# Optimization experiments

Measured on AMD Instinct MI355X. Metric: run time of the kernel, lower is better.

## Reference

```python
import jax, jax.numpy as jnp
import numpy as np

DIM, NH, HD = 1536, 12, 128
F, H, W = 1, 30, 52
SEQ = F * H * W          # 1560 tokens per AR group
NG, GI = 6, 5            # num_groups, group_idx (attend over full prefix)
POS, EPS = 1024, 1e-6


def _rope_table():
    # cos/sin table matching Wan rope_params: bands [c-2(c//3), c//3, c//3] of head_dim//2
    c = HD // 2
    parts = [c - 2 * (c // 3), c // 3, c // 3]
    pos = np.arange(POS, dtype=np.float64)
    angs = []
    for cp in parts:
        inv = 1.0 / (10000.0 ** (np.arange(cp, dtype=np.float64) / cp))
        angs.append(pos[:, None] * inv[None, :])
    ang = np.concatenate(angs, axis=1)  # [POS, c]
    return jnp.asarray(np.stack([np.cos(ang), np.sin(ang)], axis=-1), dtype=jnp.float32)


def setup_inputs() -> dict:
    key = jax.random.key(0)
    ks = jax.random.split(key, 8)
    lin = lambda k: jax.random.normal(k, (DIM, DIM), jnp.float32) * 0.02
    total = NG * SEQ
    return {
        'x': jax.random.normal(ks[0], (1, SEQ, DIM), jnp.float32),
        'wq': lin(ks[1]), 'bq': jnp.zeros((DIM,), jnp.float32),
        'wk': lin(ks[2]), 'bk': jnp.zeros((DIM,), jnp.float32),
        'wv': lin(ks[3]), 'bv': jnp.zeros((DIM,), jnp.float32),
        'wo': lin(ks[4]), 'bo': jnp.zeros((DIM,), jnp.float32),
        'nq_w': jnp.ones((DIM,), jnp.float32),
        'nk_w': jnp.ones((DIM,), jnp.float32),
        'freqs': _rope_table(),
        'k_cache': jax.random.normal(ks[5], (1, total, NH, HD), jnp.float32) * 0.5,
        'v_cache': jax.random.normal(ks[6], (1, total, NH, HD), jnp.float32) * 0.5,
        'f': F, 'h': H, 'w': W, 'group_idx': GI, 'num_groups': NG,
    }


def _rms_norm(x, weight, eps=EPS):
    # fast_rms_norm: normalize over the full channel dim, then scale
    x = x.astype(jnp.float32)
    return x * jax.lax.rsqrt(jnp.mean(x * x, axis=-1, keepdims=True) + eps) * weight


def _rope_apply(x, freqs, f, h, w, group_idx):
    # x: [B, S, N, D] with S = f*h*w; freqs: [POS, D//2, 2] (cos, sin)
    B, S, N, D = x.shape
    c = D // 2
    cf = c - 2 * (c // 3)
    ch = cw = c // 3
    sf = group_idx * f
    fp = jnp.broadcast_to(freqs[sf:sf + f, :cf][:, None, None], (f, h, w, cf, 2))
    hp = jnp.broadcast_to(freqs[:h, cf:cf + ch][None, :, None], (f, h, w, ch, 2))
    wp = jnp.broadcast_to(freqs[:w, cf + ch:][None, None, :], (f, h, w, cw, 2))
    rot = jnp.concatenate([fp, hp, wp], axis=3).reshape(S, c, 2)  # [S, c, 2]
    cos = rot[..., 0][None, :, None]  # [1, S, 1, c]
    sin = rot[..., 1][None, :, None]
    xr = x.astype(jnp.float32).reshape(B, S, N, c, 2)
    out_r = xr[..., 0] * cos - xr[..., 1] * sin  # complex multiply x * e^{i theta}
    out_i = xr[..., 0] * sin + xr[..., 1] * cos
    return jnp.stack([out_r, out_i], axis=-1).reshape(B, S, N, D)


def reference(x, wq, bq, wk, bk, wv, bv, wo, bo, nq_w, nk_w, freqs,
              k_cache, v_cache, f, h, w, group_idx, num_groups):
    B, S, C = x.shape
    n, d = NH, C // NH
    q = _rms_norm(x @ wq.T + bq, nq_w).reshape(B, S, n, d)
    k = _rms_norm(x @ wk.T + bk, nk_w).reshape(B, S, n, d)
    v = (x @ wv.T + bv).reshape(B, S, n, d)
    q = _rope_apply(q, freqs, f, h, w, group_idx)
    k = _rope_apply(k, freqs, f, h, w, group_idx)
    # KV-cache scatter (detached in the original) then prefix gather
    start = group_idx * S
    kc = jax.lax.dynamic_update_slice(k_cache, jax.lax.stop_gradient(k), (0, start, 0, 0))
    vc = jax.lax.dynamic_update_slice(v_cache, jax.lax.stop_gradient(v), (0, start, 0, 0))
    k_full = kc[:, :start + S]  # [B, Lkv, n, d]
    v_full = vc[:, :start + S]
    att = jnp.einsum('bqnd,bknd->bnqk', q, k_full) / jnp.sqrt(jnp.float32(d))
    p = jax.nn.softmax(att, axis=-1)
    o = jnp.einsum('bnqk,bknd->bqnd', p, v_full).reshape(B, S, C)
    return o @ wo.T + bo
```

## Files before the change

kernel.cpp:

```cpp
#include <hip/hip_runtime.h>

#define DIM 1536
#define NH 12
#define HD 128
#define KSPLIT 8
#define KT 32
#define MFIX 3.0f
#define KK48 48

typedef _Float16 half2_t __attribute__((ext_vector_type(2)));
typedef _Float16 half8_t __attribute__((ext_vector_type(8)));
typedef float f32x4 __attribute__((ext_vector_type(4)));

__device__ __forceinline__ half2_t pkrtz(float a, float b) {
    return __builtin_bit_cast(half2_t, __builtin_amdgcn_cvt_pkrtz(a, b));
}

__device__ __forceinline__ void split8(float4 a, float4 b, half8_t& h, half8_t& l) {
    half2_t h0 = pkrtz(a.x, a.y), h1 = pkrtz(a.z, a.w);
    half2_t h2 = pkrtz(b.x, b.y), h3 = pkrtz(b.z, b.w);
    half2_t g0 = pkrtz(a.x - (float)h0.x, a.y - (float)h0.y);
    half2_t g1 = pkrtz(a.z - (float)h1.x, a.w - (float)h1.y);
    half2_t g2 = pkrtz(b.x - (float)h2.x, b.y - (float)h2.y);
    half2_t g3 = pkrtz(b.z - (float)h3.x, b.w - (float)h3.y);
    h[0]=h0.x; h[1]=h0.y; h[2]=h1.x; h[3]=h1.y; h[4]=h2.x; h[5]=h2.y; h[6]=h3.x; h[7]=h3.y;
    l[0]=g0.x; l[1]=g0.y; l[2]=g1.x; l[3]=g1.y; l[4]=g2.x; l[5]=g2.y; l[6]=g3.x; l[7]=g3.y;
}

__device__ __forceinline__ half8_t cvt8rn(float4 a, float4 b) {
    half8_t h;
    h[0]=(_Float16)a.x; h[1]=(_Float16)a.y; h[2]=(_Float16)a.z; h[3]=(_Float16)a.w;
    h[4]=(_Float16)b.x; h[5]=(_Float16)b.y; h[6]=(_Float16)b.z; h[7]=(_Float16)b.w;
    return h;
}

__device__ __forceinline__ void gl2lds16(const void* g, void* l) {
    __builtin_amdgcn_global_load_lds(
        (const __attribute__((address_space(1))) unsigned int*)g,
        (__attribute__((address_space(3))) unsigned int*)(unsigned int)(uintptr_t)l,
        16, 0, 0);
}


__global__ __launch_bounds__(256) void cvt_a_fl(
    const float* __restrict__ src, _Float16* __restrict__ h, _Float16* __restrict__ l,
    int M, int nrec8)
{
    const int i = blockIdx.x * 256 + threadIdx.x;
    if (i >= nrec8) return;
    const int lane = i & 63;
    const int grp  = (i >> 6) & 7;
    const int tile = i >> 9;
    const int kk = tile % KK48, mt = tile / KK48;
    const int row = mt * 128 + grp * 16 + (lane & 15);
    const int k   = kk * 32 + (lane >> 4) * 8;
    float4 a = make_float4(0,0,0,0), b = a;
    if (row < M) {
        const float* s = src + (size_t)row * DIM + k;
        a = *(const float4*)s; b = *(const float4*)(s + 4);
    }
    half8_t hh, ll; split8(a, b, hh, ll);
    ((half8_t*)h)[i] = hh;
    ((half8_t*)l)[i] = ll;
}

__global__ __launch_bounds__(256) void cvt_w_fl(
    const float* __restrict__ s0, const float* __restrict__ s1,
    const float* __restrict__ s2, const float* __restrict__ s3,
    _Float16* __restrict__ h0, _Float16* __restrict__ l0,
    _Float16* __restrict__ h1, _Float16* __restrict__ l1,
    _Float16* __restrict__ h2, _Float16* __restrict__ l2,
    _Float16* __restrict__ h3, _Float16* __restrict__ l3, int nrec8)
{
    const int i = blockIdx.x * 256 + threadIdx.x;
    if (i >= nrec8) return;
    const int m = blockIdx.y;
    const float* src = m == 0 ? s0 : m == 1 ? s1 : m == 2 ? s2 : s3;
    _Float16* h = m == 0 ? h0 : m == 1 ? h1 : m == 2 ? h2 : h3;
    _Float16* l = m == 0 ? l0 : m == 1 ? l1 : m == 2 ? l2 : l3;
    const int lane = i & 63;
    const int grp  = (i >> 6) & 7;
    const int tile = i >> 9;
    const int kk = tile % KK48, nt = tile / KK48;
    const int row = nt * 128 + grp * 16 + (lane & 15);
    const int k   = kk * 32 + (lane >> 4) * 8;
    const float* s = src + (size_t)row * DIM + k;
    float4 a = *(const float4*)s, b = *(const float4*)(s + 4);
    half8_t hh, ll; split8(a, b, hh, ll);
    ((half8_t*)h)[i] = hh;
    ((half8_t*)l)[i] = ll;
}

__global__ __launch_bounds__(256) void gemm_fl(
    const _Float16* __restrict__ Ah, const _Float16* __restrict__ Al,
    const _Float16* __restrict__ Bh0, const _Float16* __restrict__ Bl0,
    const _Float16* __restrict__ Bh1, const _Float16* __restrict__ Bl1,
    const _Float16* __restrict__ Bh2, const _Float16* __restrict__ Bl2,
    const float* __restrict__ bias0, const float* __restrict__ bias1, const float* __restrict__ bias2,
    float* __restrict__ C0, float* __restrict__ C1, float* __restrict__ C2,
    int M)
{
    __shared__ __align__(16) _Float16 T[2][4][4096];

    const int MT = (M + 127) >> 7;
    const int nwg = gridDim.x;
    const int L = blockIdx.x;
    const int q8 = nwg >> 3, r8 = nwg & 7;
    const int xcd = L & 7, si = L >> 3;
    const int logical = (xcd < r8 ? xcd * (q8 + 1)
                                  : r8 * (q8 + 1) + (xcd - r8) * q8) + si;
    const int bxx = logical / MT;
    const int myy = logical % MT;
    const int mat = bxx / 12, nt = bxx % 12;
    const _Float16* Bh   = mat == 0 ? Bh0 : mat == 1 ? Bh1 : Bh2;
    const _Float16* Bl   = mat == 0 ? Bl0 : mat == 1 ? Bl1 : Bl2;
    const float*    bias = mat == 0 ? bias0 : mat == 1 ? bias1 : bias2;
    float*          C    = mat == 0 ? C0 : mat == 1 ? C1 : C2;
    const int m0 = myy * 128, n0 = nt * 128;

    const int tid = threadIdx.x;
    const int lane = tid & 63, wave = tid >> 6;
    const int l16 = lane & 15, quad = lane >> 4;
    const int wm = (wave >> 1) * 64, wn = (wave & 1) * 64;

    const _Float16* Arh = Ah + (size_t)myy * KK48 * 4096;
    const _Float16* Arl = Al + (size_t)myy * KK48 * 4096;
    const _Float16* Brh = Bh + (size_t)nt  * KK48 * 4096;
    const _Float16* Brl = Bl + (size_t)nt  * KK48 * 4096;

    f32x4 acc[4][4];
    #pragma unroll
    for (int i = 0; i < 4; ++i)
        #pragma unroll
        for (int j = 0; j < 4; ++j) acc[i][j] = (f32x4){0.f, 0.f, 0.f, 0.f};

    auto STAGE = [&](int kk, int buf) {
        const size_t off = (size_t)kk * 4096 + wave * 1024 + lane * 8;
        _Float16* d0 = &T[buf][0][wave * 1024];
        _Float16* d1 = &T[buf][1][wave * 1024];
        _Float16* d2 = &T[buf][2][wave * 1024];
        _Float16* d3 = &T[buf][3][wave * 1024];
        gl2lds16(Arh + off,       d0);
        gl2lds16(Arh + off + 512, d0 + 512);
        gl2lds16(Arl + off,       d1);
        gl2lds16(Arl + off + 512, d1 + 512);
        gl2lds16(Brh + off,       d2);
        gl2lds16(Brh + off + 512, d2 + 512);
        gl2lds16(Brl + off,       d3);
        gl2lds16(Brl + off + 512, d3 + 512);
    };

    STAGE(0, 0);
    int cur = 0;
    for (int kk = 0; kk < KK48; ++kk) {
        if (kk + 1 < KK48) {
            STAGE(kk + 1, cur ^ 1);
            asm volatile("s_waitcnt vmcnt(8)" ::: "memory");
        } else {
            asm volatile("s_waitcnt vmcnt(0)" ::: "memory");
        }
        __builtin_amdgcn_s_barrier();
        __builtin_amdgcn_sched_barrier(0);

        half8_t ah[4], al[4], bh[4], bl[4];
        const half8_t* tA = (const half8_t*)&T[cur][0][0];
        const half8_t* tAl= (const half8_t*)&T[cur][1][0];
        const half8_t* tB = (const half8_t*)&T[cur][2][0];
        const half8_t* tBl= (const half8_t*)&T[cur][3][0];
        #pragma unroll
        for (int ms = 0; ms < 4; ++ms) {
            ah[ms] = tA [((wm >> 4) + ms) * 64 + lane];
            al[ms] = tAl[((wm >> 4) + ms) * 64 + lane];
        }
        #pragma unroll
        for (int ns = 0; ns < 4; ++ns) {
            bh[ns] = tB [((wn >> 4) + ns) * 64 + lane];
            bl[ns] = tBl[((wn >> 4) + ns) * 64 + lane];
        }
        __builtin_amdgcn_s_setprio(1);
        #pragma unroll
        for (int ms = 0; ms < 4; ++ms)
            #pragma unroll
            for (int ns = 0; ns < 4; ++ns) {
                acc[ms][ns] = __builtin_amdgcn_mfma_f32_16x16x32_f16(ah[ms], bh[ns], acc[ms][ns], 0, 0, 0);
                acc[ms][ns] = __builtin_amdgcn_mfma_f32_16x16x32_f16(ah[ms], bl[ns], acc[ms][ns], 0, 0, 0);
                acc[ms][ns] = __builtin_amdgcn_mfma_f32_16x16x32_f16(al[ms], bh[ns], acc[ms][ns], 0, 0, 0);
            }
        __builtin_amdgcn_s_setprio(0);

        __builtin_amdgcn_sched_barrier(0);
        __builtin_amdgcn_s_barrier();
        cur ^= 1;
    }

    float bv[4];
    #pragma unroll
    for (int ns = 0; ns < 4; ++ns) bv[ns] = bias[n0 + wn + ns*16 + l16];
    #pragma unroll
    for (int ms = 0; ms < 4; ++ms)
        #pragma unroll
        for (int r = 0; r < 4; ++r) {
            const int row = m0 + wm + ms*16 + quad*4 + r;
            if (row < M) {
                #pragma unroll
                for (int ns = 0; ns < 4; ++ns)
                    C[(size_t)row * DIM + n0 + wn + ns*16 + l16] = acc[ms][ns][r] + bv[ns];
            }
        }
}

__global__ __launch_bounds__(256) void rms_rope2(
    float* __restrict__ qb, float* __restrict__ kb,
    const float* __restrict__ wq_, const float* __restrict__ wk_,
    const float* __restrict__ freqs,
    const int* __restrict__ fp, const int* __restrict__ hp,
    const int* __restrict__ wp, const int* __restrict__ gip)
{
    const int s = blockIdx.x;
    float* xv = blockIdx.y ? kb : qb;
    const float* w = blockIdx.y ? wk_ : wq_;
    const int tid = threadIdx.x;
    float* row = xv + (size_t)s * DIM;
    float ss = 0.f;
    for (int c = tid; c < DIM; c += 256) { float v = row[c]; ss += v * v; }
    #pragma unroll
    for (int off = 32; off > 0; off >>= 1) ss += __shfl_down(ss, off, 64);
    __shared__ float red[4];
    if ((tid & 63) == 0) red[tid >> 6] = ss;
    __syncthreads();
    const float tot = red[0] + red[1] + red[2] + red[3];
    const float scale = rsqrtf(tot / (float)DIM + 1e-6f);
    const int f = *fp, h = *hp, ww = *wp, gi = *gip;
    const int hw = h * ww;
    const int fi = s / hw;
    const int rem = s - fi * hw;
    const int hi = rem / ww;
    const int wi = rem - hi * ww;
    const int sf = gi * f;
    for (int p = tid; p < DIM / 2; p += 256) {
        int n = p >> 6, i = p & 63;
        int pos = (i < 22) ? (sf + fi) : (i < 43) ? hi : wi;
        float cs = freqs[pos * 128 + i * 2];
        float sn = freqs[pos * 128 + i * 2 + 1];
        int base = n * HD + 2 * i;
        float x0 = row[base] * scale * w[base];
        float x1 = row[base + 1] * scale * w[base + 1];
        row[base] = x0 * cs - x1 * sn;
        row[base + 1] = x0 * sn + x1 * cs;
    }
}

__global__ __launch_bounds__(256) void kv_prep(
    const float* __restrict__ kws, const float* __restrict__ kcache,
    const float* __restrict__ vws, const float* __restrict__ vcache,
    _Float16* __restrict__ KV, int S, int NT, const int* __restrict__ gip)
{
    const int t = blockIdx.x, n = blockIdx.y;
    const int tid = threadIdx.x;
    const int lane = tid & 63;
    const int l16 = lane & 15, quad = lane >> 4;
    const int start = gip[0] * S;
    const int nk = start + S;
    _Float16* outk = KV + (size_t)(n * NT + t) * 8192;
    _Float16* outv = outk + 4096;
    #pragma unroll
    for (int fi = 0; fi < 2; ++fi) {
        const int f = (tid >> 6) + fi * 4;
        const int ks = f >> 2, db = f & 3;
        const int j = t * KT + ks * 16 + l16;
        float4 a = make_float4(0,0,0,0), b = a;
        if (j < nk) {
            const float* src = (j < start) ? (kcache + (size_t)j * DIM)
                                           : (kws + (size_t)(j - start) * DIM);
            src += n * HD + db * 32 + quad * 8;
            a = *(const float4*)src;
            b = *(const float4*)(src + 4);
        }
        *(half8_t*)&outk[(f * 64 + lane) * 8] = cvt8rn(a, b);
    }
    #pragma unroll
    for (int fi = 0; fi < 2; ++fi) {
        const int ds = (tid >> 6) + fi * 4;
        const int dim = n * HD + ds * 16 + l16;
        half8_t h;
        #pragma unroll
        for (int j = 0; j < 8; ++j) {
            const int key = t * KT + quad * 8 + j;
            float v = 0.f;
            if (key < nk)
                v = (key < start) ? vcache[(size_t)key * DIM + dim]
                                  : vws[(size_t)(key - start) * DIM + dim];
            h[j] = (_Float16)v;
        }
        *(half8_t*)&outv[(ds * 64 + lane) * 8] = h;
    }
}

#define PSTRH 40
__global__ __launch_bounds__(512) void attn_mfma(
    const float* __restrict__ q,
    const _Float16* __restrict__ KV,
    float* __restrict__ Op, float* __restrict__ Ml,
    int S, int NT, const int* __restrict__ gip)
{
    __shared__ __align__(16) _Float16 T[2][8192];
    __shared__ __align__(16) _Float16 Ph[8][16][PSTRH];

    const int nwg = gridDim.x;
    const int L = blockIdx.x;
    const int q8 = nwg >> 3, r8 = nwg & 7;
    const int xcd = L & 7, si = L >> 3;
    const int logical = (xcd < r8 ? xcd * (q8 + 1)
                                  : r8 * (q8 + 1) + (xcd - r8) * q8) + si;
    const int yb = (S + 127) >> 7;
    const int y = logical % yb;
    const int g = logical / yb;
    const int n = g % NH;
    const int ksp = g / NH;
    const int q0 = y * 128;

    const int tid = threadIdx.x;
    const int wave = tid >> 6;
    const int lane = tid & 63;
    const int l16 = lane & 15;
    const int quad = lane >> 4;
    const int start = gip[0] * S;
    const int nk = start + S;
    const int totTiles = (nk + KT - 1) / KT;
    const int tilesPer = (totTiles + KSPLIT - 1) / KSPLIT;
    const int t0 = ksp * tilesPer;
    const int t1 = min(t0 + tilesPer, totTiles);
    const float sc = 0.08838834764831845f;

    half8_t qf[4];
    {
        const int qrow = q0 + wave * 16 + l16;
        const bool qv = qrow < S;
        const float* qp = q + (size_t)(qv ? qrow : 0) * DIM + n * HD + quad * 8;
        #pragma unroll
        for (int db = 0; db < 4; ++db) {
            float4 a = make_float4(0,0,0,0), b = a;
            if (qv) { a = *(const float4*)(qp + db * 32); b = *(const float4*)(qp + db * 32 + 4); }
            qf[db] = cvt8rn(a, b);
        }
    }

    half8_t ones_f;
    {
        _Float16 ov = (l16 == 0) ? (_Float16)1.0f : (_Float16)0.0f;
        #pragma unroll
        for (int j = 0; j < 8; ++j) ones_f[j] = ov;
    }

    f32x4 O[9];
    #pragma unroll
    for (int ds = 0; ds < 9; ++ds) O[ds] = (f32x4){0.f, 0.f, 0.f, 0.f};

    const size_t tb = (size_t)n * NT;

    if (t0 < t1) {
        const _Float16* gp = KV + (tb + t0) * 8192 + wave * 512 + lane * 8;
        gl2lds16(gp,        &T[0][wave * 512]);
        gl2lds16(gp + 4096, &T[0][wave * 512 + 4096]);
    }

    int cur = 0;
    for (int t = t0; t < t1; ++t) {
        if (t + 1 < t1) {
            const _Float16* gp = KV + (tb + t + 1) * 8192 + wave * 512 + lane * 8;
            _Float16* d = &T[cur ^ 1][wave * 512];
            gl2lds16(gp,        d);
            gl2lds16(gp + 4096, d + 4096);
            asm volatile("s_waitcnt vmcnt(2)" ::: "memory");
        } else {
            asm volatile("s_waitcnt vmcnt(0)" ::: "memory");
        }
        __builtin_amdgcn_s_barrier();
        __builtin_amdgcn_sched_barrier(0);

        f32x4 sacc[2];
        sacc[0] = (f32x4){0.f, 0.f, 0.f, 0.f};
        sacc[1] = (f32x4){0.f, 0.f, 0.f, 0.f};
        const half8_t* kh8 = (const half8_t*)&T[cur][0];
        __builtin_amdgcn_s_setprio(1);
        #pragma unroll
        for (int ks = 0; ks < 2; ++ks) {
            #pragma unroll
            for (int db = 0; db < 4; ++db) {
                half8_t bh = kh8[(ks * 4 + db) * 64 + lane];
                sacc[ks] = __builtin_amdgcn_mfma_f32_16x16x32_f16(qf[db], bh, sacc[ks], 0, 0, 0);
            }
        }
        __builtin_amdgcn_s_setprio(0);

        const int k0 = t * KT;
        const bool v0 = (k0 + l16) < nk;
        const bool v1 = (k0 + 16 + l16) < nk;
        #pragma unroll
        for (int r = 0; r < 4; ++r) {
            float p0 = v0 ? __expf(sacc[0][r] * sc - MFIX) : 0.f;
            float p1 = v1 ? __expf(sacc[1][r] * sc - MFIX) : 0.f;
            Ph[wave][quad * 4 + r][l16] = (_Float16)p0;
            Ph[wave][quad * 4 + r][16 + l16] = (_Float16)p1;
        }

        half8_t ph = *(const half8_t*)&Ph[wave][l16][quad * 8];

        const half8_t* vt8 = (const half8_t*)&T[cur][4096];
        __builtin_amdgcn_s_setprio(1);
        #pragma unroll
        for (int ds = 0; ds < 8; ++ds) {
            half8_t vh = vt8[ds * 64 + lane];
            O[ds] = __builtin_amdgcn_mfma_f32_16x16x32_f16(ph, vh, O[ds], 0, 0, 0);
        }
        O[8] = __builtin_amdgcn_mfma_f32_16x16x32_f16(ph, ones_f, O[8], 0, 0, 0);
        __builtin_amdgcn_s_setprio(0);

        __builtin_amdgcn_sched_barrier(0);
        __builtin_amdgcn_s_barrier();
        cur ^= 1;
    }

    #pragma unroll
    for (int r = 0; r < 4; ++r) {
        const int row = q0 + wave * 16 + quad * 4 + r;
        if (row < S) {
            float* op = Op + (((size_t)ksp * NH + n) * S + row) * HD + l16;
            #pragma unroll
            for (int ds = 0; ds < 8; ++ds) op[ds * 16] = O[ds][r];
            if (l16 == 0)
                Ml[((size_t)ksp * NH + n) * S + row] = O[8][r];
        }
    }
}

__global__ __launch_bounds__(256) void attn_merge(
    const float* __restrict__ Op, const float* __restrict__ Ml,
    _Float16* __restrict__ oh, _Float16* __restrict__ ol, int S)
{
    const int idx = blockIdx.x * 256 + threadIdx.x;
    const int total = NH * S * HD / 2;
    if (idx >= total) return;
    const int d0 = (idx & 63) * 2;
    const int t = idx >> 6;
    const int row = t % S;
    const int n = t / S;
    float num0 = 0.f, num1 = 0.f, den = 0.f;
    #pragma unroll
    for (int ks = 0; ks < KSPLIT; ++ks) {
        const size_t base = ((size_t)ks * NH + n) * S + row;
        num0 += Op[base * HD + d0];
        num1 += Op[base * HD + d0 + 1];
        den += Ml[base];
    }
    const float v0 = num0 / den, v1 = num1 / den;
    half2_t h = pkrtz(v0, v1);
    half2_t l = pkrtz(v0 - (float)h.x, v1 - (float)h.y);
    const int k = n * HD + d0;
    const int mt = row >> 7, rr = row & 127;
    const int grp = rr >> 4, l16r = rr & 15;
    const int kk = k >> 5, quad = (k & 31) >> 3, jj = k & 7;
    const size_t a = ((size_t)(mt * KK48 + kk) * 4096)
                   + ((size_t)(grp * 64 + quad * 16 + l16r) * 8) + jj;
    *(half2_t*)&oh[a] = h;
    *(half2_t*)&ol[a] = l;
}

extern "C" void kernel_launch(void* const* d_in, const int* in_sizes, int n_in,
                              void* d_out, int out_size, void* d_ws, size_t ws_size,
                              hipStream_t stream)
{
    const float* x      = (const float*)d_in[0];
    const float* wq     = (const float*)d_in[1];
    const float* bq     = (const float*)d_in[2];
    const float* wk     = (const float*)d_in[3];
    const float* bk     = (const float*)d_in[4];
    const float* wv     = (const float*)d_in[5];
    const float* bv     = (const float*)d_in[6];
    const float* wo     = (const float*)d_in[7];
    const float* bo     = (const float*)d_in[8];
    const float* nqw    = (const float*)d_in[9];
    const float* nkw    = (const float*)d_in[10];
    const float* freqs  = (const float*)d_in[11];
    const float* kcache = (const float*)d_in[12];
    const float* vcache = (const float*)d_in[13];
    const int*   fp     = (const int*)d_in[14];
    const int*   hp     = (const int*)d_in[15];
    const int*   wp     = (const int*)d_in[16];
    const int*   gip    = (const int*)d_in[17];

    const int S = in_sizes[0] / DIM;
    const int total = in_sizes[12] / (NH * HD);
    const int NT = (total + KT - 1) / KT;
    const int MT = (S + 127) / 128;
    const size_t sd = (size_t)S * DIM;
    const size_t arec = (size_t)MT * KK48 * 4096;
    const size_t wrec = (size_t)12 * KK48 * 4096;

    char* p = (char*)d_ws;
    float* q  = (float*)p;            p += sd * 4;
    float* k  = (float*)p;            p += sd * 4;
    float* v  = (float*)p;            p += sd * 4;
    float* Op = (float*)p;            p += (size_t)KSPLIT * NH * S * HD * 4;
    float* Ml = (float*)p;            p += (size_t)KSPLIT * NH * S * 4;
    _Float16* KV  = (_Float16*)p;     p += (size_t)NH * NT * 8192 * 2;
    _Float16* xh  = (_Float16*)p;     p += arec * 2;
    _Float16* xl  = (_Float16*)p;     p += arec * 2;
    _Float16* oh  = (_Float16*)p;     p += arec * 2;
    _Float16* ol  = (_Float16*)p;     p += arec * 2;
    _Float16* wqh = (_Float16*)p;     p += wrec * 2;
    _Float16* wql = (_Float16*)p;     p += wrec * 2;
    _Float16* wkh = (_Float16*)p;     p += wrec * 2;
    _Float16* wkl = (_Float16*)p;     p += wrec * 2;
    _Float16* wvh = (_Float16*)p;     p += wrec * 2;
    _Float16* wvl = (_Float16*)p;     p += wrec * 2;
    _Float16* woh = (_Float16*)p;     p += wrec * 2;
    _Float16* wol = (_Float16*)p;     p += wrec * 2;
    float* out = (float*)d_out;

    const int an8 = (int)(arec / 8), wn8 = (int)(wrec / 8);

    cvt_a_fl<<<dim3((an8 + 255) / 256), dim3(256), 0, stream>>>(x, xh, xl, S, an8);
    cvt_w_fl<<<dim3((wn8 + 255) / 256, 4), dim3(256), 0, stream>>>(
        wq, wk, wv, wo, wqh, wql, wkh, wkl, wvh, wvl, woh, wol, wn8);

    gemm_fl<<<dim3(36 * MT), dim3(256), 0, stream>>>(
        xh, xl, wqh, wql, wkh, wkl, wvh, wvl, bq, bk, bv, q, k, v, S);
    rms_rope2<<<dim3(S, 2), dim3(256), 0, stream>>>(q, k, nqw, nkw, freqs, fp, hp, wp, gip);
    kv_prep<<<dim3(NT, NH), dim3(256), 0, stream>>>(k, kcache, v, vcache, KV, S, NT, gip);
    {
        const int yb = (S + 127) / 128;
        const int nwg = NH * yb * KSPLIT;
        attn_mfma<<<dim3(nwg), dim3(512), 0, stream>>>(
            q, KV, Op, Ml, S, NT, gip);
    }
    attn_merge<<<dim3((NH * S * HD / 2 + 255) / 256), dim3(256), 0, stream>>>(Op, Ml, oh, ol, S);
    gemm_fl<<<dim3(12 * MT), dim3(256), 0, stream>>>(
        oh, ol, woh, wol, woh, wol, woh, wol, bo, bo, bo, out, out, out, S);
}
```

Baseline: 473.8 us.

## Process two query sub-tiles per wave to reuse K/V tiles in attention

Measured after the change: 547.0 us. 1.15x slower.

```diff
diff --git a/kernel.cpp b/kernel.cpp
--- a/kernel.cpp
+++ b/kernel.cpp
@@ -285,7 +285,8 @@
         half8_t h;
         #pragma unroll
         for (int j = 0; j < 8; ++j) {
-            const int key = t * KT + quad * 8 + j;
+            const int slot = quad * 8 + j;
+            const int key = t * KT + (slot >> 1) + 16 * (slot & 1);
             float v = 0.f;
             if (key < nk)
                 v = (key < start) ? vcache[(size_t)key * DIM + dim]
@@ -296,15 +297,15 @@
     }
 }
 
-#define PSTRH 40
-__global__ __launch_bounds__(512) void attn_mfma(
+#define PSTRH 36
+__global__ __launch_bounds__(512, 4) void attn_mfma(
     const float* __restrict__ q,
     const _Float16* __restrict__ KV,
     float* __restrict__ Op, float* __restrict__ Ml,
     int S, int NT, const int* __restrict__ gip)
 {
     __shared__ __align__(16) _Float16 T[2][8192];
-    __shared__ __align__(16) _Float16 Ph[8][16][PSTRH];
+    __shared__ __align__(16) _Float16 Ph[8][2][16][PSTRH];
 
     const int nwg = gridDim.x;
     const int L = blockIdx.x;
@@ -312,12 +313,12 @@
     const int xcd = L & 7, si = L >> 3;
     const int logical = (xcd < r8 ? xcd * (q8 + 1)
                                   : r8 * (q8 + 1) + (xcd - r8) * q8) + si;
-    const int yb = (S + 127) >> 7;
+    const int yb = (S + 255) >> 8;
     const int y = logical % yb;
     const int g = logical / yb;
     const int n = g % NH;
     const int ksp = g / NH;
-    const int q0 = y * 128;
+    const int q0 = y * 256;
 
     const int tid = threadIdx.x;
     const int wave = tid >> 6;
@@ -332,16 +333,17 @@
     const int t1 = min(t0 + tilesPer, totTiles);
     const float sc = 0.08838834764831845f;
 
-    half8_t qf[4];
-    {
-        const int qrow = q0 + wave * 16 + l16;
+    half8_t qf[2][4];
+    #pragma unroll
+    for (int qs = 0; qs < 2; ++qs) {
+        const int qrow = q0 + wave * 32 + qs * 16 + l16;
         const bool qv = qrow < S;
         const float* qp = q + (size_t)(qv ? qrow : 0) * DIM + n * HD + quad * 8;
         #pragma unroll
         for (int db = 0; db < 4; ++db) {
             float4 a = make_float4(0,0,0,0), b = a;
             if (qv) { a = *(const float4*)(qp + db * 32); b = *(const float4*)(qp + db * 32 + 4); }
-            qf[db] = cvt8rn(a, b);
+            qf[qs][db] = cvt8rn(a, b);
         }
     }
 
@@ -352,9 +354,11 @@
         for (int j = 0; j < 8; ++j) ones_f[j] = ov;
     }
 
-    f32x4 O[9];
-    #pragma unroll
-    for (int ds = 0; ds < 9; ++ds) O[ds] = (f32x4){0.f, 0.f, 0.f, 0.f};
+    f32x4 O[2][9];
+    #pragma unroll
+    for (int qs = 0; qs < 2; ++qs)
+        #pragma unroll
+        for (int ds = 0; ds < 9; ++ds) O[qs][ds] = (f32x4){0.f, 0.f, 0.f, 0.f};
 
     const size_t tb = (size_t)n * NT;
 
@@ -378,9 +382,12 @@
         __builtin_amdgcn_s_barrier();
         __builtin_amdgcn_sched_barrier(0);
 
-        f32x4 sacc[2];
-        sacc[0] = (f32x4){0.f, 0.f, 0.f, 0.f};
-        sacc[1] = (f32x4){0.f, 0.f, 0.f, 0.f};
+        f32x4 sacc[2][2];
+        #pragma unroll
+        for (int qs = 0; qs < 2; ++qs) {
+            sacc[qs][0] = (f32x4){0.f, 0.f, 0.f, 0.f};
+            sacc[qs][1] = (f32x4){0.f, 0.f, 0.f, 0.f};
+        }
         const half8_t* kh8 = (const half8_t*)&T[cur][0];
         __builtin_amdgcn_s_setprio(1);
         #pragma unroll
@@ -388,7 +395,8 @@
             #pragma unroll
             for (int db = 0; db < 4; ++db) {
                 half8_t bh = kh8[(ks * 4 + db) * 64 + lane];
-                sacc[ks] = __builtin_amdgcn_mfma_f32_16x16x32_f16(qf[db], bh, sacc[ks], 0, 0, 0);
+                sacc[0][ks] = __builtin_amdgcn_mfma_f32_16x16x32_f16(qf[0][db], bh, sacc[0][ks], 0, 0, 0);
+                sacc[1][ks] = __builtin_amdgcn_mfma_f32_16x16x32_f16(qf[1][db], bh, sacc[1][ks], 0, 0, 0);
             }
         }
         __builtin_amdgcn_s_setprio(0);
@@ -397,23 +405,33 @@
         const bool v0 = (k0 + l16) < nk;
         const bool v1 = (k0 + 16 + l16) < nk;
         #pragma unroll
-        for (int r = 0; r < 4; ++r) {
-            float p0 = v0 ? __expf(sacc[0][r] * sc - MFIX) : 0.f;
-            float p1 = v1 ? __expf(sacc[1][r] * sc - MFIX) : 0.f;
-            Ph[wave][quad * 4 + r][l16] = (_Float16)p0;
-            Ph[wave][quad * 4 + r][16 + l16] = (_Float16)p1;
-        }
-
-        half8_t ph = *(const half8_t*)&Ph[wave][l16][quad * 8];
+        for (int qs = 0; qs < 2; ++qs) {
+            #pragma unroll
+            for (int r = 0; r < 4; ++r) {
+                float p0 = v0 ? __expf(sacc[qs][0][r] * sc - MFIX) : 0.f;
+                float p1 = v1 ? __expf(sacc[qs][1][r] * sc - MFIX) : 0.f;
+                half2_t pp;
+                pp.x = (_Float16)p0;
+                pp.y = (_Float16)p1;
+                *(half2_t*)&Ph[wave][qs][quad * 4 + r][2 * l16] = pp;
+            }
+        }
+
+        half8_t ph[2];
+        #pragma unroll
+        for (int qs = 0; qs < 2; ++qs)
+            ph[qs] = *(const half8_t*)&Ph[wave][qs][l16][quad * 8];
 
         const half8_t* vt8 = (const half8_t*)&T[cur][4096];
         __builtin_amdgcn_s_setprio(1);
         #pragma unroll
         for (int ds = 0; ds < 8; ++ds) {
             half8_t vh = vt8[ds * 64 + lane];
-            O[ds] = __builtin_amdgcn_mfma_f32_16x16x32_f16(ph, vh, O[ds], 0, 0, 0);
-        }
-        O[8] = __builtin_amdgcn_mfma_f32_16x16x32_f16(ph, ones_f, O[8], 0, 0, 0);
+            O[0][ds] = __builtin_amdgcn_mfma_f32_16x16x32_f16(ph[0], vh, O[0][ds], 0, 0, 0);
+            O[1][ds] = __builtin_amdgcn_mfma_f32_16x16x32_f16(ph[1], vh, O[1][ds], 0, 0, 0);
+        }
+        O[0][8] = __builtin_amdgcn_mfma_f32_16x16x32_f16(ph[0], ones_f, O[0][8], 0, 0, 0);
+        O[1][8] = __builtin_amdgcn_mfma_f32_16x16x32_f16(ph[1], ones_f, O[1][8], 0, 0, 0);
         __builtin_amdgcn_s_setprio(0);
 
         __builtin_amdgcn_sched_barrier(0);
@@ -422,16 +440,18 @@
     }
 
     #pragma unroll
-    for (int r = 0; r < 4; ++r) {
-        const int row = q0 + wave * 16 + quad * 4 + r;
-        if (row < S) {
-            float* op = Op + (((size_t)ksp * NH + n) * S + row) * HD + l16;
-            #pragma unroll
-            for (int ds = 0; ds < 8; ++ds) op[ds * 16] = O[ds][r];
-            if (l16 == 0)
-                Ml[((size_t)ksp * NH + n) * S + row] = O[8][r];
-        }
-    }
+    for (int qs = 0; qs < 2; ++qs)
+        #pragma unroll
+        for (int r = 0; r < 4; ++r) {
+            const int row = q0 + wave * 32 + qs * 16 + quad * 4 + r;
+            if (row < S) {
+                float* op = Op + (((size_t)ksp * NH + n) * S + row) * HD + l16;
+                #pragma unroll
+                for (int ds = 0; ds < 8; ++ds) op[ds * 16] = O[qs][ds][r];
+                if (l16 == 0)
+                    Ml[((size_t)ksp * NH + n) * S + row] = O[qs][8][r];
+            }
+        }
 }
 
 __global__ __launch_bounds__(256) void attn_merge(
@@ -529,7 +549,7 @@
     rms_rope2<<<dim3(S, 2), dim3(256), 0, stream>>>(q, k, nqw, nkw, freqs, fp, hp, wp, gip);
     kv_prep<<<dim3(NT, NH), dim3(256), 0, stream>>>(k, kcache, v, vcache, KV, S, NT, gip);
     {
-        const int yb = (S + 127) / 128;
+        const int yb = (S + 255) / 256;
         const int nwg = NH * yb * KSPLIT;
         attn_mfma<<<dim3(nwg), dim3(512), 0, stream>>>(
             q, KV, Op, Ml, S, NT, gip);
```
